# Performance work log

Measured on AMD Instinct MI355X. Metric: run time of the kernel, lower is better.

## Reference

```python
import jax, jax.numpy as jnp
import numpy as np
import math

D = 2048
H = 8
DK = D // H // 2  # 128
NL = 3
EPS = 1e-6
SCALE = 1.0 / math.sqrt(DK)


def _ln(x, g, b):
    m = jnp.mean(x, axis=-1, keepdims=True)
    v = jnp.mean(jnp.square(x - m), axis=-1, keepdims=True)
    return (x - m) * jax.lax.rsqrt(v + EPS) * g + b


def _attn_layer(x, g, b, Wq, Wk, Wv):
    bs = x.shape[0]
    xn = _ln(x, g, b)
    # torch Linear: y = x @ W.T ; reshape to (bs, h, 2, d_k)
    q = (xn @ Wq.T).reshape(bs, H, 2, DK)
    k = (xn @ Wk.T).reshape(bs, H, 2, DK)
    v = (xn @ Wv.T).reshape(bs, H, 2, DK)
    s = jnp.einsum('bhpd,bhqd->bhpq', q, k) * SCALE  # tiny 2x2 scores
    a = jax.nn.softmax(s, axis=-1)
    o = jnp.einsum('bhpq,bhqd->bhpd', a, v).reshape(bs, D)
    return o + x


def _ff_layer(x, lnd_g, lnd_b, lnt_g, lnt_b, Wd1, bd1, Wd2, bd2, Wt1, bt1, Wt2, bt2):
    d, t = x[:, :D // 2], x[:, D // 2:]
    dn = _ln(d, lnd_g, lnd_b)
    tn = _ln(t, lnt_g, lnt_b)
    do = jax.nn.relu(dn @ Wd1.T + bd1) @ Wd2.T + bd2
    to = jax.nn.relu(tn @ Wt1.T + bt1) @ Wt2.T + bt2
    return jnp.concatenate([do, to], axis=-1) + x


def setup_inputs() -> dict:
    key = jax.random.key(0)
    ks = iter(jax.random.split(key, 64))
    s = 0.02
    inp = {}
    inp['x'] = jax.random.normal(next(ks), (8192, D), dtype=jnp.float32)
    # attention stacks: NL layers
    inp['attn_ln_g'] = jnp.ones((NL, D), jnp.float32)
    inp['attn_ln_b'] = jnp.zeros((NL, D), jnp.float32)
    inp['Wq'] = jax.random.normal(next(ks), (NL, D, D), jnp.float32) * s
    inp['Wk'] = jax.random.normal(next(ks), (NL, D, D), jnp.float32) * s
    inp['Wv'] = jax.random.normal(next(ks), (NL, D, D), jnp.float32) * s
    # feedforward stacks: NL-1 layers
    F = NL - 1
    hd = D // 2
    inp['ff_lnd_g'] = jnp.ones((F, hd), jnp.float32)
    inp['ff_lnd_b'] = jnp.zeros((F, hd), jnp.float32)
    inp['ff_lnt_g'] = jnp.ones((F, hd), jnp.float32)
    inp['ff_lnt_b'] = jnp.zeros((F, hd), jnp.float32)
    inp['Wd1'] = jax.random.normal(next(ks), (F, D, hd), jnp.float32) * s
    inp['bd1'] = jnp.zeros((F, D), jnp.float32)
    inp['Wd2'] = jax.random.normal(next(ks), (F, hd, D), jnp.float32) * s
    inp['bd2'] = jnp.zeros((F, hd), jnp.float32)
    inp['Wt1'] = jax.random.normal(next(ks), (F, D, hd), jnp.float32) * s
    inp['bt1'] = jnp.zeros((F, D), jnp.float32)
    inp['Wt2'] = jax.random.normal(next(ks), (F, hd, D), jnp.float32) * s
    inp['bt2'] = jnp.zeros((F, hd), jnp.float32)
    # output head
    inp['Wo1'] = jax.random.normal(next(ks), (hd, D), jnp.float32) * s
    inp['bo1'] = jnp.zeros((hd,), jnp.float32)
    inp['Wo2'] = jax.random.normal(next(ks), (1, hd), jnp.float32) * s
    inp['bo2'] = jnp.zeros((1,), jnp.float32)
    return inp


def reference(x, attn_ln_g, attn_ln_b, Wq, Wk, Wv,
              ff_lnd_g, ff_lnd_b, ff_lnt_g, ff_lnt_b,
              Wd1, bd1, Wd2, bd2, Wt1, bt1, Wt2, bt2,
              Wo1, bo1, Wo2, bo2):
    for n in range(NL - 1):
        x = _attn_layer(x, attn_ln_g[n], attn_ln_b[n], Wq[n], Wk[n], Wv[n])
        x = _ff_layer(x, ff_lnd_g[n], ff_lnd_b[n], ff_lnt_g[n], ff_lnt_b[n],
                      Wd1[n], bd1[n], Wd2[n], bd2[n], Wt1[n], bt1[n], Wt2[n], bt2[n])
    x = _attn_layer(x, attn_ln_g[-1], attn_ln_b[-1], Wq[-1], Wk[-1], Wv[-1])
    h = jax.nn.relu(x @ Wo1.T + bo1)
    return h @ Wo2.T + bo2  # [bs, 1]
```

## Files before the change

kernel.cpp:

```cpp
#include <hip/hip_runtime.h>
#include <stdint.h>


typedef __bf16 bf16x8 __attribute__((ext_vector_type(8)));
typedef float f32x4 __attribute__((ext_vector_type(4)));

static __device__ __forceinline__ float bf2f(unsigned short u) {
  unsigned int x = ((unsigned int)u) << 16;
  float f;
  __builtin_memcpy(&f, &x, 4);
  return f;
}
static __device__ __forceinline__ unsigned short f2bf(float f) {
  unsigned int x;
  __builtin_memcpy(&x, &f, 4);
  x += 0x7fffu + ((x >> 16) & 1u);
  return (unsigned short)(x >> 16);
}

static __device__ __forceinline__ void gload_lds16(const void* g, void* l) {
  __builtin_amdgcn_global_load_lds(
      (const __attribute__((address_space(1))) unsigned int*)g,
      (__attribute__((address_space(3))) unsigned int*)l, 16, 0, 0);
}

__global__ __launch_bounds__(256) void cvt_kernel(
    const float* __restrict__ in, unsigned short* __restrict__ out, long n) {
  const long i = ((long)blockIdx.x * 256 + threadIdx.x) * 4;
  if (i + 3 < n) {
    float4 f = *(const float4*)(in + i);
    *(ushort4*)(out + i) = make_ushort4(f2bf(f.x), f2bf(f.y), f2bf(f.z), f2bf(f.w));
  }
}

#define MAXSEG 14
struct CvtArgs {
  const float* src[MAXSEG];
  unsigned short* dst[MAXSEG];
  long pfx[MAXSEG + 1];
  int ns;
};
__global__ __launch_bounds__(256) void cvt_multi_kernel(CvtArgs a) {
  const long i = ((long)blockIdx.x * 256 + threadIdx.x) * 4;
  int s = 0;
  while (s + 1 < a.ns && i >= a.pfx[s + 1]) ++s;
  const long off = i - a.pfx[s];
  float4 f = *(const float4*)(a.src[s] + off);
  *(ushort4*)(a.dst[s] + off) =
      make_ushort4(f2bf(f.x), f2bf(f.y), f2bf(f.z), f2bf(f.w));
}

#define BARRIER __builtin_amdgcn_s_barrier()
#define LGKM(N)                                                     \
  do {                                                              \
    asm volatile("s_waitcnt lgkmcnt(" #N ")" ::: "memory");         \
    __builtin_amdgcn_sched_barrier(0);                              \
  } while (0)
#define VMC(N)                                                      \
  do {                                                              \
    asm volatile("s_waitcnt vmcnt(" #N ")" ::: "memory");           \
    __builtin_amdgcn_sched_barrier(0);                              \
  } while (0)

__global__ __launch_bounds__(512, 4) void gemm2b_kernel(
    const unsigned short* __restrict__ A, int lda,
    const unsigned short* __restrict__ B, int K,
    void* __restrict__ Cp, int ldc, const float* __restrict__ bias,
    int relu, int out_f32, int resadd,
    const unsigned short* __restrict__ A2, const unsigned short* __restrict__ B2,
    void* __restrict__ C2p, const float* __restrict__ bias2, int dual) {
  __shared__ __align__(16) char smem[49152];

  const int tid = threadIdx.x;
  const int lane = tid & 63;
  const int w = tid >> 6;
  const int wm = w >> 1;
  const int wn = w & 1;
  const long brow = (long)blockIdx.y * 256;

  const unsigned short* Ap = A;
  const unsigned short* Bp = B;
  const float* bi = bias;
  void* Cq = Cp;
  long bcol;
  const int gx = (int)gridDim.x;
  const int bx = (int)blockIdx.x;
  if (dual && bx >= (gx >> 1)) {
    Ap = A2; Bp = B2; bi = bias2; Cq = C2p;
    bcol = (long)(bx - (gx >> 1)) * 128;
  } else {
    bcol = (long)bx * 128;
  }

  const int NT = K >> 6;

  const int lrA = tid >> 3;
  const int scb = ((tid & 7) * 16) ^ (((tid >> 3) & 7) << 4);
  const unsigned wb = (unsigned)tid * 16;
  const long ldab = (long)lda * 2;
  const long ldbb = (long)K * 2;
  const char* gA = (const char*)Ap + (brow + lrA) * ldab + scb;
  const char* gB = (const char*)Bp + (bcol + lrA) * ldbb + scb;
  const long a64 = 64 * ldab, a128 = 128 * ldab, a192 = 192 * ldab;
  const long b64 = 64 * ldbb;

#define STAGE(off)                                              \
  do {                                                          \
    gload_lds16(gA + (off), smem + (wb & ~1023u));              \
    gload_lds16(gA + a64 + (off), smem + 8192 + (wb & ~1023u)); \
    gload_lds16(gA + a128 + (off), smem + 16384 + (wb & ~1023u)); \
    gload_lds16(gA + a192 + (off), smem + 24576 + (wb & ~1023u)); \
    gload_lds16(gB + (off), smem + 32768 + (wb & ~1023u));      \
    gload_lds16(gB + b64 + (off), smem + 40960 + (wb & ~1023u)); \
  } while (0)

  f32x4 acc[4][4];
  const f32x4 fz = {0.f, 0.f, 0.f, 0.f};
#pragma unroll
  for (int m = 0; m < 4; ++m)
#pragma unroll
    for (int n = 0; n < 4; ++n) acc[m][n] = fz;

  const int frow = lane & 15;
  const int fkb = (lane >> 4) * 16;
  const int fswz = (lane & 7) << 4;

#define RDA(dst, M, KK)                                                       \
  dst = *(const bf16x8*)(smem + (wm * 64 + (M) * 16 + frow) * 128 +           \
                         (((KK) * 64 + fkb) ^ fswz))
#define RDB(dst, N, KK)                                                       \
  dst = *(const bf16x8*)(smem + 32768 + (wn * 64 + (N) * 16 + frow) * 128 +   \
                         (((KK) * 64 + fkb) ^ fswz))

#define MM16(A4, B4)                                                          \
  do {                                                                        \
    _Pragma("unroll") for (int mm = 0; mm < 4; ++mm)                          \
    _Pragma("unroll") for (int nn = 0; nn < 4; ++nn)                          \
        acc[mm][nn] = __builtin_amdgcn_mfma_f32_16x16x32_bf16(                \
            A4[mm], B4[nn], acc[mm][nn], 0, 0, 0);                            \
  } while (0)

  STAGE(0);
  long soff = 128;

  for (int t = 0; t < NT; ++t) {
    VMC(0);
    BARRIER;

    bf16x8 a0[4], b0[4];
    RDA(a0[0], 0, 0); RDA(a0[1], 1, 0); RDA(a0[2], 2, 0); RDA(a0[3], 3, 0);
    RDB(b0[0], 0, 0); RDB(b0[1], 1, 0); RDB(b0[2], 2, 0); RDB(b0[3], 3, 0);
    LGKM(0);
    __builtin_amdgcn_s_setprio(1);
    MM16(a0, b0);
    __builtin_amdgcn_s_setprio(0);
    __builtin_amdgcn_sched_barrier(0);

    bf16x8 a1[4], b1[4];
    RDA(a1[0], 0, 1); RDA(a1[1], 1, 1); RDA(a1[2], 2, 1); RDA(a1[3], 3, 1);
    RDB(b1[0], 0, 1); RDB(b1[1], 1, 1); RDB(b1[2], 2, 1); RDB(b1[3], 3, 1);
    LGKM(0);
    BARRIER;
    if (t + 1 < NT) STAGE(soff);
    __builtin_amdgcn_s_setprio(1);
    MM16(a1, b1);
    __builtin_amdgcn_s_setprio(0);
    __builtin_amdgcn_sched_barrier(0);
    soff += 128;
  }

  const long rb0 = brow + wm * 64 + (lane >> 4) * 4;
  const long cb0 = bcol + wn * 64 + (lane & 15);
#pragma unroll
  for (int m = 0; m < 4; ++m) {
#pragma unroll
    for (int n = 0; n < 4; ++n) {
      const long col = cb0 + n * 16;
      const float bv = bi ? bi[col] : 0.f;
#pragma unroll
      for (int j = 0; j < 4; ++j) {
        const long r = rb0 + m * 16 + j;
        float v = acc[m][n][j] + bv;
        if (relu) v = fmaxf(v, 0.f);
        if (out_f32) {
          float* cp = (float*)Cq + r * (long)ldc + col;
          if (resadd) v += *cp;
          *cp = v;
        } else {
          unsigned short* cp = (unsigned short*)Cq + r * (long)ldc + col;
          if (resadd) v += bf2f(*cp);
          *cp = f2bf(v);
        }
      }
    }
  }
#undef STAGE
#undef RDA
#undef RDB
#undef MM16
}

__global__ __launch_bounds__(256) void gemm_bt_kernel(
    const unsigned short* __restrict__ A, int lda,
    const unsigned short* __restrict__ B, int K,
    void* __restrict__ Cp, int ldc,
    const float* __restrict__ bias,
    const void* __restrict__ res, int res_mode, int ldres,
    int relu, int out_f32) {
  __shared__ __align__(16) unsigned short As[128 * 32];
  __shared__ __align__(16) unsigned short Bs[128 * 32];

  const int t = threadIdx.x;
  const int lane = t & 63;
  const int w = t >> 6;
  const int wr = (w >> 1) * 64;
  const int wc = (w & 1) * 64;
  const long brow = (long)blockIdx.y * 128;
  const long bcol = (long)blockIdx.x * 128;

  const int srow = lane >> 2;
  const int scol = (lane & 3) * 8;
  const unsigned short* Ab = A + (brow + w * 32 + srow) * (long)lda + scol;
  const unsigned short* Bb = B + (bcol + w * 32 + srow) * (long)K + scol;
  unsigned short* Asb = &As[(w * 32) * 32];
  unsigned short* Bsb = &Bs[(w * 32) * 32];

  f32x4 acc[4][4];
  const f32x4 fzero = {0.f, 0.f, 0.f, 0.f};
#pragma unroll
  for (int m = 0; m < 4; ++m)
#pragma unroll
    for (int n = 0; n < 4; ++n) acc[m][n] = fzero;

  const int fr = lane & 15;
  const int fk = (lane >> 4) * 8;

  for (int kt = 0; kt < K; kt += 32) {
    gload_lds16(Ab + kt, Asb);
    gload_lds16(Ab + 16 * (long)lda + kt, Asb + 16 * 32);
    gload_lds16(Bb + kt, Bsb);
    gload_lds16(Bb + 16 * (long)K + kt, Bsb + 16 * 32);
    __syncthreads();

    bf16x8 af[4], bfv[4];
#pragma unroll
    for (int m = 0; m < 4; ++m)
      af[m] = *(const bf16x8*)&As[(wr + m * 16 + fr) * 32 + fk];
#pragma unroll
    for (int n = 0; n < 4; ++n)
      bfv[n] = *(const bf16x8*)&Bs[(wc + n * 16 + fr) * 32 + fk];
#pragma unroll
    for (int m = 0; m < 4; ++m)
#pragma unroll
      for (int n = 0; n < 4; ++n)
        acc[m][n] = __builtin_amdgcn_mfma_f32_16x16x32_bf16(af[m], bfv[n],
                                                            acc[m][n], 0, 0, 0);
    __syncthreads();
  }

  const long rbase = brow + wr + (lane >> 4) * 4;
#pragma unroll
  for (int m = 0; m < 4; ++m) {
#pragma unroll
    for (int n = 0; n < 4; ++n) {
      const long col = bcol + wc + n * 16 + fr;
      const float bv = bias ? bias[col] : 0.f;
#pragma unroll
      for (int j = 0; j < 4; ++j) {
        const long r = rbase + m * 16 + j;
        float v = acc[m][n][j] + bv;
        if (relu) v = fmaxf(v, 0.f);
        if (res_mode == 1)
          v += ((const float*)res)[r * (long)ldres + col];
        else if (res_mode == 2)
          v += bf2f(((const unsigned short*)res)[r * (long)ldres + col]);
        if (out_f32)
          ((float*)Cp)[r * (long)ldc + col] = v;
        else
          ((unsigned short*)Cp)[r * (long)ldc + col] = f2bf(v);
      }
    }
  }
}

template <int L>
__global__ __launch_bounds__(256) void ln_kernel(
    const void* __restrict__ inp, int in_bf16, int ldin,
    const float* __restrict__ g, const float* __restrict__ b,
    unsigned short* __restrict__ outp, int ldout) {
  constexpr int VEC = L / 256;
  const long row = blockIdx.x;
  const int t = threadIdx.x;
  float v[VEC];
  if (in_bf16) {
    const unsigned short* p = (const unsigned short*)inp + row * (long)ldin + t * VEC;
#pragma unroll
    for (int i = 0; i < VEC; i += 4) {
      ushort4 u = *(const ushort4*)(p + i);
      v[i] = bf2f(u.x); v[i + 1] = bf2f(u.y); v[i + 2] = bf2f(u.z); v[i + 3] = bf2f(u.w);
    }
  } else {
    const float* p = (const float*)inp + row * (long)ldin + t * VEC;
#pragma unroll
    for (int i = 0; i < VEC; i += 4) {
      float4 f = *(const float4*)(p + i);
      v[i] = f.x; v[i + 1] = f.y; v[i + 2] = f.z; v[i + 3] = f.w;
    }
  }
  float s = 0.f, sq = 0.f;
#pragma unroll
  for (int i = 0; i < VEC; ++i) { s += v[i]; sq += v[i] * v[i]; }
#pragma unroll
  for (int off = 32; off; off >>= 1) {
    s += __shfl_xor(s, off, 64);
    sq += __shfl_xor(sq, off, 64);
  }
  __shared__ float red[8];
  if ((t & 63) == 0) { red[t >> 6] = s; red[4 + (t >> 6)] = sq; }
  __syncthreads();
  s = red[0] + red[1] + red[2] + red[3];
  sq = red[4] + red[5] + red[6] + red[7];
  const float mean = s * (1.f / L);
  const float var = sq * (1.f / L) - mean * mean;
  const float rstd = rsqrtf(var + 1e-6f);
  unsigned short* op = outp + row * (long)ldout + t * VEC;
  const float* gp = g + t * VEC;
  const float* bp = b + t * VEC;
#pragma unroll
  for (int i = 0; i < VEC; i += 4) {
    float4 gg = *(const float4*)(gp + i);
    float4 bb = *(const float4*)(bp + i);
    *(ushort4*)(op + i) = make_ushort4(
        f2bf((v[i + 0] - mean) * rstd * gg.x + bb.x),
        f2bf((v[i + 1] - mean) * rstd * gg.y + bb.y),
        f2bf((v[i + 2] - mean) * rstd * gg.z + bb.z),
        f2bf((v[i + 3] - mean) * rstd * gg.w + bb.w));
  }
}

__global__ __launch_bounds__(512) void attn_glue_kernel(
    const unsigned short* __restrict__ Q, const unsigned short* __restrict__ Kq,
    const unsigned short* __restrict__ V, int ld, const void* __restrict__ Xres,
    int res_bf16, void* __restrict__ Xout, int out_bf16,
    unsigned short* __restrict__ Xout_bf,
    unsigned short* __restrict__ DNp, unsigned short* __restrict__ TNp,
    const float* __restrict__ lnd_g, const float* __restrict__ lnd_b,
    const float* __restrict__ lnt_g, const float* __restrict__ lnt_b) {
  const long row = blockIdx.x;
  const int h = threadIdx.x >> 6;
  const int lane = threadIdx.x & 63;
  const long qbase = row * (long)ld + h * 256;
  const long xbase = row * 2048 + h * 256;
  const int d = lane * 2;

  ushort2 q0 = *(const ushort2*)&Q[qbase + d];
  ushort2 q1 = *(const ushort2*)&Q[qbase + 128 + d];
  ushort2 k0 = *(const ushort2*)&Kq[qbase + d];
  ushort2 k1 = *(const ushort2*)&Kq[qbase + 128 + d];
  ushort2 v0 = *(const ushort2*)&V[qbase + d];
  ushort2 v1 = *(const ushort2*)&V[qbase + 128 + d];

  const float q0x = bf2f(q0.x), q0y = bf2f(q0.y);
  const float q1x = bf2f(q1.x), q1y = bf2f(q1.y);
  const float k0x = bf2f(k0.x), k0y = bf2f(k0.y);
  const float k1x = bf2f(k1.x), k1y = bf2f(k1.y);

  float s00 = q0x * k0x + q0y * k0y;
  float s01 = q0x * k1x + q0y * k1y;
  float s10 = q1x * k0x + q1y * k0y;
  float s11 = q1x * k1x + q1y * k1y;
#pragma unroll
  for (int off = 32; off; off >>= 1) {
    s00 += __shfl_xor(s00, off, 64);
    s01 += __shfl_xor(s01, off, 64);
    s10 += __shfl_xor(s10, off, 64);
    s11 += __shfl_xor(s11, off, 64);
  }
  const float SC = 0.088388347648318447f;
  s00 *= SC; s01 *= SC; s10 *= SC; s11 *= SC;
  const float m0 = fmaxf(s00, s01), m1 = fmaxf(s10, s11);
  const float e00 = __expf(s00 - m0), e01 = __expf(s01 - m0);
  const float e10 = __expf(s10 - m1), e11 = __expf(s11 - m1);
  const float i0 = 1.f / (e00 + e01), i1 = 1.f / (e10 + e11);
  const float a00 = e00 * i0, a01 = e01 * i0;
  const float a10 = e10 * i1, a11 = e11 * i1;

  const float v0x = bf2f(v0.x), v0y = bf2f(v0.y);
  const float v1x = bf2f(v1.x), v1y = bf2f(v1.y);
  float o0x = a00 * v0x + a01 * v1x, o0y = a00 * v0y + a01 * v1y;
  float o1x = a10 * v0x + a11 * v1x, o1y = a10 * v0y + a11 * v1y;

  if (res_bf16) {
    const unsigned short* xr = (const unsigned short*)Xres + xbase;
    ushort2 ra = *(const ushort2*)&xr[d];
    ushort2 rb = *(const ushort2*)&xr[128 + d];
    o0x += bf2f(ra.x); o0y += bf2f(ra.y); o1x += bf2f(rb.x); o1y += bf2f(rb.y);
  } else {
    const float* xr = (const float*)Xres + xbase;
    float2 ra = *(const float2*)&xr[d];
    float2 rb = *(const float2*)&xr[128 + d];
    o0x += ra.x; o0y += ra.y; o1x += rb.x; o1y += rb.y;
  }
  if (Xout) {
    if (out_bf16) {
      unsigned short* xo = (unsigned short*)Xout + xbase;
      *(ushort2*)&xo[d] = make_ushort2(f2bf(o0x), f2bf(o0y));
      *(ushort2*)&xo[128 + d] = make_ushort2(f2bf(o1x), f2bf(o1y));
    } else {
      float* xo = (float*)Xout + xbase;
      *(float2*)&xo[d] = make_float2(o0x, o0y);
      *(float2*)&xo[128 + d] = make_float2(o1x, o1y);
    }
  }
  if (Xout_bf) {
    unsigned short* xb = Xout_bf + xbase;
    *(ushort2*)&xb[d] = make_ushort2(f2bf(o0x), f2bf(o0y));
    *(ushort2*)&xb[128 + d] = make_ushort2(f2bf(o1x), f2bf(o1y));
  }

  if (DNp) {
    float s4 = o0x + o0y + o1x + o1y;
    float q4 = o0x * o0x + o0y * o0y + o1x * o1x + o1y * o1y;
#pragma unroll
    for (int off = 32; off; off >>= 1) {
      s4 += __shfl_xor(s4, off, 64);
      q4 += __shfl_xor(q4, off, 64);
    }
    __shared__ float redS[8], redQ[8];
    if (lane == 0) { redS[h] = s4; redQ[h] = q4; }
    __syncthreads();
    const int b4 = (h >> 2) * 4;
    const float S = redS[b4] + redS[b4 + 1] + redS[b4 + 2] + redS[b4 + 3];
    const float Qs = redQ[b4] + redQ[b4 + 1] + redQ[b4 + 2] + redQ[b4 + 3];
    const float mean = S * (1.f / 1024.f);
    const float var = Qs * (1.f / 1024.f) - mean * mean;
    const float rstd = rsqrtf(var + 1e-6f);
    const float* gp = (h < 4) ? lnd_g : lnt_g;
    const float* bp = (h < 4) ? lnd_b : lnt_b;
    unsigned short* dst = ((h < 4) ? DNp : TNp) + row * 1024;
    const int hc = (h & 3) * 256 + d;
    float2 g0 = *(const float2*)&gp[hc];
    float2 b0 = *(const float2*)&bp[hc];
    *(ushort2*)&dst[hc] = make_ushort2(f2bf((o0x - mean) * rstd * g0.x + b0.x),
                                       f2bf((o0y - mean) * rstd * g0.y + b0.y));
    float2 g1 = *(const float2*)&gp[hc + 128];
    float2 b1 = *(const float2*)&bp[hc + 128];
    *(ushort2*)&dst[hc + 128] =
        make_ushort2(f2bf((o1x - mean) * rstd * g1.x + b1.x),
                     f2bf((o1y - mean) * rstd * g1.y + b1.y));
  }
}

__global__ __launch_bounds__(256) void final_matvec_kernel(
    const unsigned short* __restrict__ Hm, const float* __restrict__ wv,
    const float* __restrict__ b2, float* __restrict__ outp) {
  const long row = blockIdx.x;
  const int t = threadIdx.x;
  ushort4 hv = *(const ushort4*)&Hm[row * 1024 + t * 4];
  float4 wq = *(const float4*)&wv[t * 4];
  float s = bf2f(hv.x) * wq.x + bf2f(hv.y) * wq.y +
            bf2f(hv.z) * wq.z + bf2f(hv.w) * wq.w;
#pragma unroll
  for (int off = 32; off; off >>= 1) s += __shfl_xor(s, off, 64);
  __shared__ float red[4];
  if ((t & 63) == 0) red[t >> 6] = s;
  __syncthreads();
  if (t == 0) outp[row] = red[0] + red[1] + red[2] + red[3] + b2[0];
}

extern "C" void kernel_launch(void* const* d_in, const int* in_sizes, int n_in,
                              void* d_out, int out_size, void* d_ws,
                              size_t ws_size, hipStream_t stream) {
  const float* x_in = (const float*)d_in[0];
  const float* aln_g = (const float*)d_in[1];
  const float* aln_b = (const float*)d_in[2];
  const float* Wq_f = (const float*)d_in[3];
  const float* Wk_f = (const float*)d_in[4];
  const float* Wv_f = (const float*)d_in[5];
  const float* lnd_g = (const float*)d_in[6];
  const float* lnd_b = (const float*)d_in[7];
  const float* lnt_g = (const float*)d_in[8];
  const float* lnt_b = (const float*)d_in[9];
  const float* Wd1_f = (const float*)d_in[10];
  const float* bd1 = (const float*)d_in[11];
  const float* Wd2_f = (const float*)d_in[12];
  const float* bd2 = (const float*)d_in[13];
  const float* Wt1_f = (const float*)d_in[14];
  const float* bt1 = (const float*)d_in[15];
  const float* Wt2_f = (const float*)d_in[16];
  const float* bt2 = (const float*)d_in[17];
  const float* Wo1_f = (const float*)d_in[18];
  const float* bo1 = (const float*)d_in[19];
  const float* Wo2_f = (const float*)d_in[20];
  const float* bo2 = (const float*)d_in[21];

  const size_t R = 8192, D = 2048, HD = 1024;
  const size_t DD = D * D;
  const size_t WALL = (3 * 3 * DD + 4 * 2 * D * HD + HD * D) * 2;
  const size_t SLOT = 3 * DD * 2;
  const size_t ACT = R * D * 4 + R * D * 2 + R * 6144 * 2;

  auto cvt = [&](const float* src, unsigned short* dst, long n) {
    cvt_kernel<<<dim3((unsigned)(n / 1024)), dim3(256), 0, stream>>>(src, dst, n);
  };

  if (ws_size >= ACT + SLOT) {
    const bool planAll = ws_size >= ACT + WALL;

    char* p = (char*)d_ws;
    unsigned short* Xb = (unsigned short*)p; p += R * D * 4;
    unsigned short* XN = (unsigned short*)p; p += R * D * 2;
    unsigned short* QKVb = (unsigned short*)p; p += R * 6144 * 2;
    unsigned short* Warea = (unsigned short*)p;

    unsigned short* H1d = QKVb;
    unsigned short* H1t = QKVb + R * 2048;
    unsigned short* Hfin = QKVb + R * 4096;
    unsigned short* DN = XN;
    unsigned short* TN = XN + R * HD;

    unsigned short* Wqkv_b = Warea;
    unsigned short* Wd1_b = Wqkv_b + 9 * DD;
    unsigned short* Wt1_b = Wd1_b + 2 * D * HD;
    unsigned short* Wd2_b = Wt1_b + 2 * D * HD;
    unsigned short* Wt2_b = Wd2_b + 2 * D * HD;
    unsigned short* Wo1_b = Wt2_b + 2 * D * HD;
    if (planAll) {
      CvtArgs ca;
      int s = 0;
      long pfx = 0;
      auto add = [&](const float* src, unsigned short* dst, long n) {
        ca.src[s] = src; ca.dst[s] = dst; ca.pfx[s] = pfx; pfx += n; ++s;
      };
      for (int n = 0; n < 3; ++n) {
        add(Wq_f + n * DD, Wqkv_b + n * 3 * DD + 0 * DD, (long)DD);
        add(Wk_f + n * DD, Wqkv_b + n * 3 * DD + 1 * DD, (long)DD);
        add(Wv_f + n * DD, Wqkv_b + n * 3 * DD + 2 * DD, (long)DD);
      }
      add(Wd1_f, Wd1_b, (long)(2 * D * HD));
      add(Wt1_f, Wt1_b, (long)(2 * D * HD));
      add(Wd2_f, Wd2_b, (long)(2 * D * HD));
      add(Wt2_f, Wt2_b, (long)(2 * D * HD));
      add(Wo1_f, Wo1_b, (long)(HD * D));
      ca.pfx[s] = pfx;
      ca.ns = s;
      cvt_multi_kernel<<<dim3((unsigned)(pfx / 1024)), dim3(256), 0, stream>>>(ca);
    }

    auto gemm = [&](const unsigned short* A, int lda, const unsigned short* B,
                    int N, int K, void* C, int ldc, const float* bias,
                    int relu, int of32, int resadd, const unsigned short* A2,
                    const unsigned short* B2, void* C2, const float* bias2) {
      const int dual = (A2 != nullptr);
      dim3 grid((dual ? 2 : 1) * (N / 128), 32);
      gemm2b_kernel<<<grid, dim3(512), 0, stream>>>(
          A, lda, B, K, C, ldc, bias, relu, of32, resadd, A2, B2, C2, bias2,
          dual);
    };

    for (int n = 0; n < 3; ++n) {
      ln_kernel<2048><<<8192, 256, 0, stream>>>(
          (n == 0) ? (const void*)x_in : (const void*)Xb, n != 0, 2048,
          aln_g + n * D, aln_b + n * D, XN, 2048);
      const unsigned short* Wqkv;
      if (planAll) {
        Wqkv = Wqkv_b + (size_t)n * 3 * DD;
      } else {
        cvt(Wq_f + n * DD, Warea + 0 * DD, DD);
        cvt(Wk_f + n * DD, Warea + 1 * DD, DD);
        cvt(Wv_f + n * DD, Warea + 2 * DD, DD);
        Wqkv = Warea;
      }
      gemm(XN, 2048, Wqkv, 6144, 2048, QKVb, 6144, nullptr, 0, 0, 0,
           nullptr, nullptr, nullptr, nullptr);
      attn_glue_kernel<<<8192, 512, 0, stream>>>(
          QKVb, QKVb + 2048, QKVb + 4096, 6144,
          (n == 0) ? (const void*)x_in : (const void*)Xb, n != 0,
          (void*)Xb, 1, nullptr,
          (n < 2) ? DN : nullptr, (n < 2) ? TN : nullptr,
          (n < 2) ? lnd_g + n * HD : nullptr, (n < 2) ? lnd_b + n * HD : nullptr,
          (n < 2) ? lnt_g + n * HD : nullptr, (n < 2) ? lnt_b + n * HD : nullptr);

      if (n < 2) {
        const size_t fo = (size_t)n * D * HD;
        const unsigned short *w1d, *w1t, *w2d, *w2t;
        if (planAll) {
          w1d = Wd1_b + fo; w1t = Wt1_b + fo; w2d = Wd2_b + fo; w2t = Wt2_b + fo;
        } else {
          cvt(Wd1_f + fo, Warea + 0 * D * HD, D * HD);
          cvt(Wt1_f + fo, Warea + 1 * D * HD, D * HD);
          cvt(Wd2_f + fo, Warea + 2 * D * HD, D * HD);
          cvt(Wt2_f + fo, Warea + 3 * D * HD, D * HD);
          w1d = Warea; w1t = Warea + D * HD; w2d = Warea + 2 * D * HD;
          w2t = Warea + 3 * D * HD;
        }
        gemm(DN, 1024, w1d, 2048, 1024, H1d, 2048, bd1 + n * D, 1, 0, 0,
             TN, w1t, H1t, bt1 + n * D);
        gemm(H1d, 2048, w2d, 1024, 2048, Xb, 2048, bd2 + n * HD, 0, 0, 1,
             H1t, w2t, Xb + HD, bt2 + n * HD);
      }
    }

    const unsigned short* Wo1p;
    if (planAll) {
      Wo1p = Wo1_b;
    } else {
      cvt(Wo1_f, Warea, HD * D);
      Wo1p = Warea;
    }
    gemm(Xb, 2048, Wo1p, 1024, 2048, Hfin, 1024, bo1, 1, 0, 0,
         nullptr, nullptr, nullptr, nullptr);
    final_matvec_kernel<<<8192, 256, 0, stream>>>(Hfin, Wo2_f, bo2,
                                                  (float*)d_out);
    return;
  }

  const size_t PLB = R * D * 2;
  const size_t XFZ = R * D * 4;
  const size_t SLOT1 = DD * 2;
  const bool planAll = ws_size >= XFZ + 4 * PLB + WALL;
  const bool xIsF32 = planAll || ws_size >= XFZ + 4 * PLB + SLOT1;

  char* p = (char*)d_ws;
  float* Xf = nullptr;
  unsigned short* Xbb = nullptr;
  if (xIsF32) { Xf = (float*)p; p += XFZ; } else { Xbb = (unsigned short*)p; p += PLB; }
  unsigned short* XN = (unsigned short*)p; p += PLB;
  unsigned short* Qb = (unsigned short*)p; p += PLB;
  unsigned short* Kb = (unsigned short*)p; p += PLB;
  unsigned short* Vb = (unsigned short*)p; p += PLB;
  unsigned short* Warea = (unsigned short*)p;

  void* X = xIsF32 ? (void*)Xf : (void*)Xbb;
  const int xres_mode = xIsF32 ? 1 : 2;
  unsigned short* H1 = Qb;
  unsigned short* DN = XN;
  unsigned short* TN = XN + R * HD;
  unsigned short* Hfin = Vb;

  unsigned short* Wq_b = Warea;
  unsigned short* Wk_b = Wq_b + 3 * DD;
  unsigned short* Wv_b = Wk_b + 3 * DD;
  unsigned short* Wd1_b = Wv_b + 3 * DD;
  unsigned short* Wd2_b = Wd1_b + 2 * D * HD;
  unsigned short* Wt1_b = Wd2_b + 2 * D * HD;
  unsigned short* Wt2_b = Wt1_b + 2 * D * HD;
  unsigned short* Wo1_b = Wt2_b + 2 * D * HD;
  if (planAll) {
    cvt(Wq_f, Wq_b, 3 * DD);
    cvt(Wk_f, Wk_b, 3 * DD);
    cvt(Wv_f, Wv_b, 3 * DD);
    cvt(Wd1_f, Wd1_b, 2 * D * HD);
    cvt(Wd2_f, Wd2_b, 2 * D * HD);
    cvt(Wt1_f, Wt1_b, 2 * D * HD);
    cvt(Wt2_f, Wt2_b, 2 * D * HD);
    cvt(Wo1_f, Wo1_b, HD * D);
  }
  auto wbf = [&](const float* src_base, unsigned short* pre_base, size_t off,
                 size_t cnt) -> const unsigned short* {
    if (planAll) return pre_base + off;
    cvt(src_base + off, Warea, (long)cnt);
    return Warea;
  };
  auto gemm = [&](const unsigned short* A, int lda, const unsigned short* B,
                  int N, int K, void* C, int ldc, const float* bias,
                  const void* res, int res_mode, int ldres, int relu, int of32) {
    dim3 grid(N / 128, 8192 / 128);
    gemm_bt_kernel<<<grid, dim3(256), 0, stream>>>(
        A, lda, B, K, C, ldc, bias, res, res_mode, ldres, relu, of32);
  };

  for (int n = 0; n < 3; ++n) {
    const void* lin = (n == 0) ? (const void*)x_in : (const void*)X;
    const int lin_bf16 = (n == 0) ? 0 : (xIsF32 ? 0 : 1);
    ln_kernel<2048><<<8192, 256, 0, stream>>>(lin, lin_bf16, 2048,
                                              aln_g + n * D, aln_b + n * D, XN, 2048);
    const size_t wo = (size_t)n * DD;
    gemm(XN, 2048, wbf(Wq_f, Wq_b, wo, DD), 2048, 2048, Qb, 2048,
         nullptr, nullptr, 0, 0, 0, 0);
    gemm(XN, 2048, wbf(Wk_f, Wk_b, wo, DD), 2048, 2048, Kb, 2048,
         nullptr, nullptr, 0, 0, 0, 0);
    gemm(XN, 2048, wbf(Wv_f, Wv_b, wo, DD), 2048, 2048, Vb, 2048,
         nullptr, nullptr, 0, 0, 0, 0);
    attn_glue_kernel<<<8192, 512, 0, stream>>>(
        Qb, Kb, Vb, 2048, (n == 0) ? (const void*)x_in : (const void*)X,
        (n == 0) ? 0 : (xIsF32 ? 0 : 1), X, xIsF32 ? 0 : 1,
        (n == 2 && xIsF32) ? XN : nullptr,
        nullptr, nullptr, nullptr, nullptr, nullptr, nullptr);

    if (n < 2) {
      const size_t fo = (size_t)n * D * HD;
      ln_kernel<1024><<<8192, 256, 0, stream>>>(X, !xIsF32, 2048,
                                                lnd_g + n * HD, lnd_b + n * HD, DN, 1024);
      const void* Xt = xIsF32 ? (const void*)(Xf + HD) : (const void*)(Xbb + HD);
      ln_kernel<1024><<<8192, 256, 0, stream>>>(Xt, !xIsF32, 2048,
                                                lnt_g + n * HD, lnt_b + n * HD, TN, 1024);
      void* Xd2 = X;
      void* Xt2 = xIsF32 ? (void*)(Xf + HD) : (void*)(Xbb + HD);
      gemm(DN, 1024, wbf(Wd1_f, Wd1_b, fo, D * HD), 2048, 1024, H1, 2048,
           bd1 + n * D, nullptr, 0, 0, 1, 0);
      gemm(H1, 2048, wbf(Wd2_f, Wd2_b, fo, D * HD), 1024, 2048, Xd2, 2048,
           bd2 + n * HD, Xd2, xres_mode, 2048, 0, xIsF32 ? 1 : 0);
      gemm(TN, 1024, wbf(Wt1_f, Wt1_b, fo, D * HD), 2048, 1024, H1, 2048,
           bt1 + n * D, nullptr, 0, 0, 1, 0);
      gemm(H1, 2048, wbf(Wt2_f, Wt2_b, fo, D * HD), 1024, 2048, Xt2, 2048,
           bt2 + n * HD, Xt2, xres_mode, 2048, 0, xIsF32 ? 1 : 0);
    }
  }

  const unsigned short* Afin = xIsF32 ? XN : Xbb;
  gemm(Afin, 2048, wbf(Wo1_f, Wo1_b, 0, HD * D), 1024, 2048, Hfin, 1024,
       bo1, nullptr, 0, 0, 1, 0);
  final_matvec_kernel<<<8192, 256, 0, stream>>>(Hfin, Wo2_f, bo2, (float*)d_out);
}
```

Measured before the change: 1.195 ms.

## Fuse fp32-to-bf16 weight conversion into GEMM B-tile loading

Removes the separate weight conversion pass (cvt_multi_kernel and per-layer cvt calls). The GEMM now reads fp32 weights straight into registers, converts them to bf16 in-kernel and writes them into swizzled LDS, with a register prefetch one tile ahead and an extra barrier per iteration. The QKV GEMM selects among the separate Wq/Wk/Wv pointers by column segment, so the weights never need to be concatenated. This saves the conversion traffic and a workspace area but doubles B global bytes per GEMM tile, adds conversion ALU work in the main loop, and shrinks the residual buffer to bf16.

```diff
diff --git a/kernel.cpp b/kernel.cpp
--- a/kernel.cpp
+++ b/kernel.cpp
@@ -31,23 +31,6 @@
     float4 f = *(const float4*)(in + i);
     *(ushort4*)(out + i) = make_ushort4(f2bf(f.x), f2bf(f.y), f2bf(f.z), f2bf(f.w));
   }
-}
-
-#define MAXSEG 14
-struct CvtArgs {
-  const float* src[MAXSEG];
-  unsigned short* dst[MAXSEG];
-  long pfx[MAXSEG + 1];
-  int ns;
-};
-__global__ __launch_bounds__(256) void cvt_multi_kernel(CvtArgs a) {
-  const long i = ((long)blockIdx.x * 256 + threadIdx.x) * 4;
-  int s = 0;
-  while (s + 1 < a.ns && i >= a.pfx[s + 1]) ++s;
-  const long off = i - a.pfx[s];
-  float4 f = *(const float4*)(a.src[s] + off);
-  *(ushort4*)(a.dst[s] + off) =
-      make_ushort4(f2bf(f.x), f2bf(f.y), f2bf(f.z), f2bf(f.w));
 }
 
 #define BARRIER __builtin_amdgcn_s_barrier()
@@ -62,12 +45,13 @@
     __builtin_amdgcn_sched_barrier(0);                              \
   } while (0)
 
-__global__ __launch_bounds__(512, 4) void gemm2b_kernel(
+__global__ __launch_bounds__(512, 4) void gemm2c_kernel(
     const unsigned short* __restrict__ A, int lda,
-    const unsigned short* __restrict__ B, int K,
+    const float* __restrict__ B0, const float* __restrict__ B1,
+    const float* __restrict__ B2, int seg, int K,
     void* __restrict__ Cp, int ldc, const float* __restrict__ bias,
     int relu, int out_f32, int resadd,
-    const unsigned short* __restrict__ A2, const unsigned short* __restrict__ B2,
+    const unsigned short* __restrict__ A2, const float* __restrict__ Bs2,
     void* __restrict__ C2p, const float* __restrict__ bias2, int dual) {
   __shared__ __align__(16) char smem[49152];
 
@@ -79,39 +63,65 @@
   const long brow = (long)blockIdx.y * 256;
 
   const unsigned short* Ap = A;
-  const unsigned short* Bp = B;
   const float* bi = bias;
   void* Cq = Cp;
-  long bcol;
+  const float* Bbase;
+  long bcol, browB;
   const int gx = (int)gridDim.x;
   const int bx = (int)blockIdx.x;
   if (dual && bx >= (gx >> 1)) {
-    Ap = A2; Bp = B2; bi = bias2; Cq = C2p;
+    Ap = A2; bi = bias2; Cq = C2p;
     bcol = (long)(bx - (gx >> 1)) * 128;
+    Bbase = Bs2;
+    browB = bcol;
   } else {
     bcol = (long)bx * 128;
+    const int idx = (bcol >= 2 * (long)seg) ? 2 : (bcol >= (long)seg ? 1 : 0);
+    Bbase = (idx == 0) ? B0 : (idx == 1 ? B1 : B2);
+    browB = bcol - (long)idx * seg;
   }
 
   const int NT = K >> 6;
 
   const int lrA = tid >> 3;
   const int scb = ((tid & 7) * 16) ^ (((tid >> 3) & 7) << 4);
-  const unsigned wb = (unsigned)tid * 16;
+  const unsigned wb = (unsigned)tid * 16 & ~1023u;
   const long ldab = (long)lda * 2;
-  const long ldbb = (long)K * 2;
   const char* gA = (const char*)Ap + (brow + lrA) * ldab + scb;
-  const char* gB = (const char*)Bp + (bcol + lrA) * ldbb + scb;
   const long a64 = 64 * ldab, a128 = 128 * ldab, a192 = 192 * ldab;
-  const long b64 = 64 * ldbb;
-
-#define STAGE(off)                                              \
+
+#define STAGE_A(off)                                      \
+  do {                                                    \
+    gload_lds16(gA + (off), smem + wb);                   \
+    gload_lds16(gA + a64 + (off), smem + 8192 + wb);      \
+    gload_lds16(gA + a128 + (off), smem + 16384 + wb);    \
+    gload_lds16(gA + a192 + (off), smem + 24576 + wb);    \
+  } while (0)
+
+  const int rB = tid >> 2;
+  const int c0 = (tid & 3) * 32;
+  const int swzB = (rB & 7) << 4;
+  char* ldsB0 = smem + 32768 + rB * 128 + (c0 ^ swzB);
+  char* ldsB1 = smem + 32768 + rB * 128 + ((c0 + 16) ^ swzB);
+  const char* gB = (const char*)Bbase + (browB + rB) * (long)K * 4 + c0 * 2;
+
+  f32x4 bregs[4];
+#define LOAD_B(toff)                                            \
   do {                                                          \
-    gload_lds16(gA + (off), smem + (wb & ~1023u));              \
-    gload_lds16(gA + a64 + (off), smem + 8192 + (wb & ~1023u)); \
-    gload_lds16(gA + a128 + (off), smem + 16384 + (wb & ~1023u)); \
-    gload_lds16(gA + a192 + (off), smem + 24576 + (wb & ~1023u)); \
-    gload_lds16(gB + (off), smem + 32768 + (wb & ~1023u));      \
-    gload_lds16(gB + b64 + (off), smem + 40960 + (wb & ~1023u)); \
+    const char* s = gB + (toff);                                \
+    bregs[0] = *(const f32x4*)(s);                              \
+    bregs[1] = *(const f32x4*)(s + 16);                         \
+    bregs[2] = *(const f32x4*)(s + 32);                         \
+    bregs[3] = *(const f32x4*)(s + 48);                         \
+  } while (0)
+#define CVT_WRITE_B()                                           \
+  do {                                                          \
+    unsigned short h[16];                                       \
+    _Pragma("unroll") for (int q = 0; q < 4; ++q)               \
+    _Pragma("unroll") for (int e = 0; e < 4; ++e)               \
+        h[q * 4 + e] = f2bf(bregs[q][e]);                       \
+    *(bf16x8*)ldsB0 = *(bf16x8*)&h[0];                          \
+    *(bf16x8*)ldsB1 = *(bf16x8*)&h[8];                          \
   } while (0)
 
   f32x4 acc[4][4];
@@ -140,12 +150,18 @@
             A4[mm], B4[nn], acc[mm][nn], 0, 0, 0);                            \
   } while (0)
 
-  STAGE(0);
-  long soff = 128;
+  LOAD_B(0);
+  STAGE_A(0);
+  VMC(4);
+  CVT_WRITE_B();
+  VMC(0);
+  LGKM(0);
+  BARRIER;
+  long soffA = 128;
+  long soffB = 256;
 
   for (int t = 0; t < NT; ++t) {
-    VMC(0);
-    BARRIER;
+    if (t + 1 < NT) LOAD_B(soffB);
 
     bf16x8 a0[4], b0[4];
     RDA(a0[0], 0, 0); RDA(a0[1], 1, 0); RDA(a0[2], 2, 0); RDA(a0[3], 3, 0);
@@ -161,12 +177,20 @@
     RDB(b1[0], 0, 1); RDB(b1[1], 1, 1); RDB(b1[2], 2, 1); RDB(b1[3], 3, 1);
     LGKM(0);
     BARRIER;
-    if (t + 1 < NT) STAGE(soff);
+    if (t + 1 < NT) {
+      STAGE_A(soffA);
+      VMC(4);
+      CVT_WRITE_B();
+    }
     __builtin_amdgcn_s_setprio(1);
     MM16(a1, b1);
     __builtin_amdgcn_s_setprio(0);
     __builtin_amdgcn_sched_barrier(0);
-    soff += 128;
+    VMC(0);
+    LGKM(0);
+    BARRIER;
+    soffA += 128;
+    soffB += 256;
   }
 
   const long rb0 = brow + wm * 64 + (lane >> 4) * 4;
@@ -194,7 +218,9 @@
       }
     }
   }
-#undef STAGE
+#undef STAGE_A
+#undef LOAD_B
+#undef CVT_WRITE_B
 #undef RDA
 #undef RDB
 #undef MM16
@@ -497,21 +523,17 @@
   const size_t R = 8192, D = 2048, HD = 1024;
   const size_t DD = D * D;
   const size_t WALL = (3 * 3 * DD + 4 * 2 * D * HD + HD * D) * 2;
-  const size_t SLOT = 3 * DD * 2;
-  const size_t ACT = R * D * 4 + R * D * 2 + R * 6144 * 2;
+  const size_t ACT = R * D * 2 + R * D * 2 + R * 6144 * 2;
 
   auto cvt = [&](const float* src, unsigned short* dst, long n) {
     cvt_kernel<<<dim3((unsigned)(n / 1024)), dim3(256), 0, stream>>>(src, dst, n);
   };
 
-  if (ws_size >= ACT + SLOT) {
-    const bool planAll = ws_size >= ACT + WALL;
-
+  if (ws_size >= ACT + (4 << 20)) {
     char* p = (char*)d_ws;
-    unsigned short* Xb = (unsigned short*)p; p += R * D * 4;
+    unsigned short* Xb = (unsigned short*)p; p += R * D * 2;
     unsigned short* XN = (unsigned short*)p; p += R * D * 2;
     unsigned short* QKVb = (unsigned short*)p; p += R * 6144 * 2;
-    unsigned short* Warea = (unsigned short*)p;
 
     unsigned short* H1d = QKVb;
     unsigned short* H1t = QKVb + R * 2048;
@@ -519,59 +541,24 @@
     unsigned short* DN = XN;
     unsigned short* TN = XN + R * HD;
 
-    unsigned short* Wqkv_b = Warea;
-    unsigned short* Wd1_b = Wqkv_b + 9 * DD;
-    unsigned short* Wt1_b = Wd1_b + 2 * D * HD;
-    unsigned short* Wd2_b = Wt1_b + 2 * D * HD;
-    unsigned short* Wt2_b = Wd2_b + 2 * D * HD;
-    unsigned short* Wo1_b = Wt2_b + 2 * D * HD;
-    if (planAll) {
-      CvtArgs ca;
-      int s = 0;
-      long pfx = 0;
-      auto add = [&](const float* src, unsigned short* dst, long n) {
-        ca.src[s] = src; ca.dst[s] = dst; ca.pfx[s] = pfx; pfx += n; ++s;
-      };
-      for (int n = 0; n < 3; ++n) {
-        add(Wq_f + n * DD, Wqkv_b + n * 3 * DD + 0 * DD, (long)DD);
-        add(Wk_f + n * DD, Wqkv_b + n * 3 * DD + 1 * DD, (long)DD);
-        add(Wv_f + n * DD, Wqkv_b + n * 3 * DD + 2 * DD, (long)DD);
-      }
-      add(Wd1_f, Wd1_b, (long)(2 * D * HD));
-      add(Wt1_f, Wt1_b, (long)(2 * D * HD));
-      add(Wd2_f, Wd2_b, (long)(2 * D * HD));
-      add(Wt2_f, Wt2_b, (long)(2 * D * HD));
-      add(Wo1_f, Wo1_b, (long)(HD * D));
-      ca.pfx[s] = pfx;
-      ca.ns = s;
-      cvt_multi_kernel<<<dim3((unsigned)(pfx / 1024)), dim3(256), 0, stream>>>(ca);
-    }
-
-    auto gemm = [&](const unsigned short* A, int lda, const unsigned short* B,
-                    int N, int K, void* C, int ldc, const float* bias,
-                    int relu, int of32, int resadd, const unsigned short* A2,
-                    const unsigned short* B2, void* C2, const float* bias2) {
+    auto gemm = [&](const unsigned short* A, int lda, const float* B0,
+                    const float* B1, const float* B2, int seg, int N, int K,
+                    void* C, int ldc, const float* bias, int relu, int of32,
+                    int resadd, const unsigned short* A2, const float* Bs2,
+                    void* C2, const float* bias2) {
       const int dual = (A2 != nullptr);
       dim3 grid((dual ? 2 : 1) * (N / 128), 32);
-      gemm2b_kernel<<<grid, dim3(512), 0, stream>>>(
-          A, lda, B, K, C, ldc, bias, relu, of32, resadd, A2, B2, C2, bias2,
-          dual);
+      gemm2c_kernel<<<grid, dim3(512), 0, stream>>>(
+          A, lda, B0, B1, B2, seg, K, C, ldc, bias, relu, of32, resadd,
+          A2, Bs2, C2, bias2, dual);
     };
 
     for (int n = 0; n < 3; ++n) {
       ln_kernel<2048><<<8192, 256, 0, stream>>>(
           (n == 0) ? (const void*)x_in : (const void*)Xb, n != 0, 2048,
           aln_g + n * D, aln_b + n * D, XN, 2048);
-      const unsigned short* Wqkv;
-      if (planAll) {
-        Wqkv = Wqkv_b + (size_t)n * 3 * DD;
-      } else {
-        cvt(Wq_f + n * DD, Warea + 0 * DD, DD);
-        cvt(Wk_f + n * DD, Warea + 1 * DD, DD);
-        cvt(Wv_f + n * DD, Warea + 2 * DD, DD);
-        Wqkv = Warea;
-      }
-      gemm(XN, 2048, Wqkv, 6144, 2048, QKVb, 6144, nullptr, 0, 0, 0,
+      gemm(XN, 2048, Wq_f + n * DD, Wk_f + n * DD, Wv_f + n * DD, 2048,
+           6144, 2048, QKVb, 6144, nullptr, 0, 0, 0,
            nullptr, nullptr, nullptr, nullptr);
       attn_glue_kernel<<<8192, 512, 0, stream>>>(
           QKVb, QKVb + 2048, QKVb + 4096, 6144,
@@ -583,33 +570,16 @@
 
       if (n < 2) {
         const size_t fo = (size_t)n * D * HD;
-        const unsigned short *w1d, *w1t, *w2d, *w2t;
-        if (planAll) {
-          w1d = Wd1_b + fo; w1t = Wt1_b + fo; w2d = Wd2_b + fo; w2t = Wt2_b + fo;
-        } else {
-          cvt(Wd1_f + fo, Warea + 0 * D * HD, D * HD);
-          cvt(Wt1_f + fo, Warea + 1 * D * HD, D * HD);
-          cvt(Wd2_f + fo, Warea + 2 * D * HD, D * HD);
-          cvt(Wt2_f + fo, Warea + 3 * D * HD, D * HD);
-          w1d = Warea; w1t = Warea + D * HD; w2d = Warea + 2 * D * HD;
-          w2t = Warea + 3 * D * HD;
-        }
-        gemm(DN, 1024, w1d, 2048, 1024, H1d, 2048, bd1 + n * D, 1, 0, 0,
-             TN, w1t, H1t, bt1 + n * D);
-        gemm(H1d, 2048, w2d, 1024, 2048, Xb, 2048, bd2 + n * HD, 0, 0, 1,
-             H1t, w2t, Xb + HD, bt2 + n * HD);
+        gemm(DN, 1024, Wd1_f + fo, nullptr, nullptr, 1 << 28, 2048, 1024,
+             H1d, 2048, bd1 + n * D, 1, 0, 0, TN, Wt1_f + fo, H1t, bt1 + n * D);
+        gemm(H1d, 2048, Wd2_f + fo, nullptr, nullptr, 1 << 28, 1024, 2048,
+             Xb, 2048, bd2 + n * HD, 0, 0, 1, H1t, Wt2_f + fo, Xb + HD,
+             bt2 + n * HD);
       }
     }
 
-    const unsigned short* Wo1p;
-    if (planAll) {
-      Wo1p = Wo1_b;
-    } else {
-      cvt(Wo1_f, Warea, HD * D);
-      Wo1p = Warea;
-    }
-    gemm(Xb, 2048, Wo1p, 1024, 2048, Hfin, 1024, bo1, 1, 0, 0,
-         nullptr, nullptr, nullptr, nullptr);
+    gemm(Xb, 2048, Wo1_f, nullptr, nullptr, 1 << 28, 1024, 2048, Hfin, 1024,
+         bo1, 1, 0, 0, nullptr, nullptr, nullptr, nullptr);
     final_matvec_kernel<<<8192, 256, 0, stream>>>(Hfin, Wo2_f, bo2,
                                                   (float*)d_out);
     return;
```

Result: slower. 3.861 ms (+223.0%).
